# Kernel tuning notes

Measured on AMD Instinct MI355X. Metric: run time of the kernel, lower is better.

Reference implementation:

```python
import jax, jax.numpy as jnp
import numpy as np

GRID = 20            # divide = [20,20,20], hard-coded in the torch module
MIN_COORD = 10.0     # -min_voxel_coord = floor(20/2)
R = GRID * GRID * GRID  # 8000 voxels per batch element


def setup_inputs() -> dict:
    key = jax.random.key(0)
    k1, k2 = jax.random.split(key)
    B, C, N = 16, 64, 65536
    features = jax.random.normal(k1, (B, C, N), dtype=jnp.float32)
    # points spread over roughly [-30, 30] so voxel indices cover the grid
    coords = jax.random.normal(k2, (B, N, 3), dtype=jnp.float32) * 10.0
    # search_area = 40 -> voxel_size = 40/20 = 2
    search_area = jnp.ones((B, 3), dtype=jnp.float32) * 40.0
    return {"features": features, "coords": coords, "search_area": search_area}


def reference(features, coords, search_area):
    # features: [B, C, N], coords: [B, N, 3], search_area: [B, 3]
    B, C, N = features.shape
    voxel_size = search_area / GRID                     # [B, 3]
    # coords.detach() in torch -> stop_gradient here
    disc = jnp.floor(jax.lax.stop_gradient(coords) / voxel_size[:, None, :])
    idx = (disc + MIN_COORD).astype(jnp.int32)          # [B, N, 3]
    idx = jnp.clip(idx, 0, GRID - 1)
    # flat voxel index within a batch element, then offset per batch
    flat = idx[..., 0] * (GRID * GRID) + idx[..., 1] * GRID + idx[..., 2]  # [B, N]
    seg = (flat + jnp.arange(B, dtype=jnp.int32)[:, None] * R).reshape(-1)  # [B*N]
    feat_flat = features.transpose(0, 2, 1).reshape(B * N, C)               # [B*N, C]
    sums = jax.ops.segment_sum(feat_flat, seg, num_segments=B * R)          # [B*R, C]
    counts = jax.ops.segment_sum(jnp.ones((B * N,), features.dtype), seg,
                                 num_segments=B * R)                        # [B*R]
    avg = sums / jnp.maximum(counts, 1.0)[:, None]
    # -> [B, C, X, Y, Z]
    return avg.reshape(B, GRID, GRID, GRID, C).transpose(0, 4, 1, 2, 3)
```

## Files before the change

### kernel.cpp

```cpp
#include <hip/hip_runtime.h>

#define GRID_D 20
#define RVOX   8000
#define BDIM   16
#define CDIM   64
#define NPTS   65536
#define NSEG   (BDIM * RVOX)
#define NPT_TOT (BDIM * NPTS)

#define FP_SCALE  1048576.0f
#define FP_BIAS_S 16777216.0f
#define FP_INV_S  9.5367431640625e-07f

__device__ __forceinline__ void lds_fadd64(unsigned off, unsigned long long v) {
    asm volatile("ds_add_u64 %0, %1" :: "v"(off), "v"(v));
}

__device__ __forceinline__ unsigned long long pack2(float a, float b) {
    unsigned lo = (unsigned)fmaf(a, FP_SCALE, FP_BIAS_S);
    unsigned hi = (unsigned)fmaf(b, FP_SCALE, FP_BIAS_S);
    return ((unsigned long long)hi << 32) | (unsigned long long)lo;
}

__global__ __launch_bounds__(256) void k_seg(
    const float* __restrict__ coords, const float* __restrict__ search_area,
    unsigned short* __restrict__ seg_idx, unsigned int* __restrict__ hist)
{
    int gid = blockIdx.x * 256 + threadIdx.x;
    int b = gid >> 16;
    int n = gid & (NPTS - 1);

    const float inv_grid = 1.0f / (float)GRID_D;
    float vsx = search_area[b * 3 + 0] * inv_grid;
    float vsy = search_area[b * 3 + 1] * inv_grid;
    float vsz = search_area[b * 3 + 2] * inv_grid;
    const float* cp = coords + (size_t)b * NPTS * 3 + (size_t)n * 3;
    int ix = (int)(floorf(cp[0] / vsx) + 10.0f);
    int iy = (int)(floorf(cp[1] / vsy) + 10.0f);
    int iz = (int)(floorf(cp[2] / vsz) + 10.0f);
    ix = min(max(ix, 0), GRID_D - 1);
    iy = min(max(iy, 0), GRID_D - 1);
    iz = min(max(iz, 0), GRID_D - 1);
    int flat = ix * (GRID_D * GRID_D) + iy * GRID_D + iz;
    seg_idx[gid] = (unsigned short)flat;
    atomicAdd(&hist[b * RVOX + flat], 1u);
}

__global__ __launch_bounds__(512) void k_accum2(
    const float* __restrict__ features,
    const unsigned short* __restrict__ seg_idx,
    const unsigned int* __restrict__ hist,
    float* __restrict__ out)
{
    extern __shared__ unsigned long long s64[];
    int tid = threadIdx.x;
    int cp = blockIdx.x;
    int b  = blockIdx.y;

    unsigned int* sz = (unsigned int*)s64;
    for (int i = tid; i < RVOX * 2; i += 512) sz[i] = 0u;
    __syncthreads();

    const float* fA = features + ((size_t)(b * CDIM + 2 * cp)) * NPTS;
    const float* fB = fA + NPTS;
    const unsigned short* sp = seg_idx + (size_t)b * NPTS;

    const int ITER = NPTS / (512 * 4);
    int p = tid * 4;
    ushort4 sg = *reinterpret_cast<const ushort4*>(sp + p);
    float4  va = *reinterpret_cast<const float4*>(fA + p);
    float4  vb = *reinterpret_cast<const float4*>(fB + p);
    for (int it = 0; it < ITER; ++it) {
        ushort4 sgn = sg;
        float4  van = va, vbn = vb;
        int pn = p + 2048;
        if (it + 1 < ITER) {
            sgn = *reinterpret_cast<const ushort4*>(sp + pn);
            van = *reinterpret_cast<const float4*>(fA + pn);
            vbn = *reinterpret_cast<const float4*>(fB + pn);
        }
        lds_fadd64((unsigned)sg.x * 8u, pack2(va.x, vb.x));
        lds_fadd64((unsigned)sg.y * 8u, pack2(va.y, vb.y));
        lds_fadd64((unsigned)sg.z * 8u, pack2(va.z, vb.z));
        lds_fadd64((unsigned)sg.w * 8u, pack2(va.w, vb.w));
        sg = sgn; va = van; vb = vbn; p = pn;
    }
    asm volatile("s_waitcnt lgkmcnt(0)");
    __syncthreads();

    const unsigned int* hb = hist + b * RVOX;
    float* oA = out + ((size_t)(b * CDIM + 2 * cp)) * RVOX;
    float* oB = oA + RVOX;
    for (int i = tid; i < RVOX / 4; i += 512) {
        int v = i * 4;
        uint4 h4 = *reinterpret_cast<const uint4*>(hb + v);
        float4 ra, rb;
        {
            unsigned long long w;
            float cnt, inv, t;
#define UNPACK(J, HJ, RA, RB)                                        \
            w = s64[v + J];                                          \
            cnt = (float)(HJ);                                       \
            inv = 1.0f / fmaxf(cnt, 1.0f);                           \
            t = cnt * -16.0f;                                        \
            RA = fmaf((float)(unsigned)w, FP_INV_S, t) * inv;        \
            RB = fmaf((float)(unsigned)(w >> 32), FP_INV_S, t) * inv;
            UNPACK(0, h4.x, ra.x, rb.x)
            UNPACK(1, h4.y, ra.y, rb.y)
            UNPACK(2, h4.z, ra.z, rb.z)
            UNPACK(3, h4.w, ra.w, rb.w)
#undef UNPACK
        }
        *reinterpret_cast<float4*>(oA + v) = ra;
        *reinterpret_cast<float4*>(oB + v) = rb;
    }
}

__global__ __launch_bounds__(256) void voxel_scatter(
    const float* __restrict__ features, const float* __restrict__ coords,
    const float* __restrict__ search_area, float* __restrict__ sums,
    float* __restrict__ counts)
{
    int gid = blockIdx.x * blockDim.x + threadIdx.x;
    int b = gid >> 16;
    int n = gid & (NPTS - 1);
    const float inv_grid = 1.0f / (float)GRID_D;
    float vsx = search_area[b * 3 + 0] * inv_grid;
    float vsy = search_area[b * 3 + 1] * inv_grid;
    float vsz = search_area[b * 3 + 2] * inv_grid;
    const float* cp = coords + (size_t)b * NPTS * 3 + (size_t)n * 3;
    int ix = (int)(floorf(cp[0] / vsx) + 10.0f);
    int iy = (int)(floorf(cp[1] / vsy) + 10.0f);
    int iz = (int)(floorf(cp[2] / vsz) + 10.0f);
    ix = min(max(ix, 0), GRID_D - 1);
    iy = min(max(iy, 0), GRID_D - 1);
    iz = min(max(iz, 0), GRID_D - 1);
    int flat = ix * (GRID_D * GRID_D) + iy * GRID_D + iz;
    atomicAdd(&counts[b * RVOX + flat], 1.0f);
    const float* fbase = features + (size_t)b * CDIM * NPTS + n;
    float* obase = sums + (size_t)b * CDIM * RVOX + flat;
#pragma unroll 8
    for (int c = 0; c < CDIM; ++c)
        atomicAdd(obase + (size_t)c * RVOX, fbase[(size_t)c * NPTS]);
}

__global__ __launch_bounds__(256) void voxel_finalize(
    float* __restrict__ out, const float* __restrict__ counts)
{
    int gid = blockIdx.x * blockDim.x + threadIdx.x;
    int i = gid * 4;
    int b = i / (CDIM * RVOX);
    int r = i % RVOX;
    float4 s = reinterpret_cast<float4*>(out)[gid];
    float4 cnt = reinterpret_cast<const float4*>(counts)[(b * RVOX + r) >> 2];
    s.x = s.x / fmaxf(cnt.x, 1.0f);
    s.y = s.y / fmaxf(cnt.y, 1.0f);
    s.z = s.z / fmaxf(cnt.z, 1.0f);
    s.w = s.w / fmaxf(cnt.w, 1.0f);
    reinterpret_cast<float4*>(out)[gid] = s;
}

extern "C" void kernel_launch(void* const* d_in, const int* in_sizes, int n_in,
                              void* d_out, int out_size, void* d_ws, size_t ws_size,
                              hipStream_t stream) {
    const float* features    = (const float*)d_in[0];
    const float* coords      = (const float*)d_in[1];
    const float* search_area = (const float*)d_in[2];
    float* out = (float*)d_out;

    unsigned short* seg_idx = (unsigned short*)d_ws;
    unsigned int* hist = (unsigned int*)((char*)d_ws + (size_t)NPT_TOT * sizeof(unsigned short));
    size_t need = (size_t)NPT_TOT * 2 + (size_t)NSEG * 4 + 256;

    if (ws_size >= need) {
        hipMemsetAsync(hist, 0, (size_t)NSEG * sizeof(unsigned int), stream);
        k_seg<<<NPT_TOT / 256, 256, 0, stream>>>(coords, search_area, seg_idx, hist);
        dim3 agrid(CDIM / 2, BDIM);
        k_accum2<<<agrid, 512, RVOX * sizeof(unsigned long long), stream>>>(
            features, seg_idx, hist, out);
    } else {
        float* counts = (float*)d_ws;
        hipMemsetAsync(out, 0, (size_t)out_size * sizeof(float), stream);
        hipMemsetAsync(counts, 0, (size_t)NSEG * sizeof(float), stream);
        voxel_scatter<<<NPT_TOT / 256, 256, 0, stream>>>(
            features, coords, search_area, out, counts);
        int nvec = (BDIM * CDIM * RVOX) / 4;
        voxel_finalize<<<(nvec + 255) / 256, 256, 0, stream>>>(out, counts);
    }
}
```

Before: 441.7 us.

## Split channel pairs between LDS atomics and global 64-bit atomics per block

Each block now handles two channel pairs. One pair is accumulated with fixed-point 64-bit LDS atomics as before, and the other with 64-bit global atomics into a zeroed workspace buffer, which a new finalize kernel then normalizes. This halves the block count to 256 at 1024 threads, and each block reads each point's segment index once for four channels. The cost is heavy global atomic traffic, a larger memset, and an extra kernel launch.

After: 1.070 ms. 142% more time.

```diff
diff --git a/kernel.cpp b/kernel.cpp
--- a/kernel.cpp
+++ b/kernel.cpp
@@ -7,6 +7,7 @@
 #define NPTS   65536
 #define NSEG   (BDIM * RVOX)
 #define NPT_TOT (BDIM * NPTS)
+#define NPAIR  16
 
 #define FP_SCALE  1048576.0f
 #define FP_BIAS_S 16777216.0f
@@ -46,53 +47,65 @@
     atomicAdd(&hist[b * RVOX + flat], 1u);
 }
 
-__global__ __launch_bounds__(512) void k_accum2(
+__global__ __launch_bounds__(1024) void k_hyb(
     const float* __restrict__ features,
     const unsigned short* __restrict__ seg_idx,
     const unsigned int* __restrict__ hist,
+    unsigned long long* __restrict__ gsum,
     float* __restrict__ out)
 {
     extern __shared__ unsigned long long s64[];
     int tid = threadIdx.x;
-    int cp = blockIdx.x;
-    int b  = blockIdx.y;
+    int i = blockIdx.x & (NPAIR - 1);
+    int b = blockIdx.x >> 4;
 
     unsigned int* sz = (unsigned int*)s64;
-    for (int i = tid; i < RVOX * 2; i += 512) sz[i] = 0u;
+    for (int k = tid; k < RVOX * 2; k += 1024) sz[k] = 0u;
     __syncthreads();
 
-    const float* fA = features + ((size_t)(b * CDIM + 2 * cp)) * NPTS;
+    const float* fA = features + ((size_t)(b * CDIM + 2 * i)) * NPTS;
     const float* fB = fA + NPTS;
+    const float* fC = features + ((size_t)(b * CDIM + 2 * NPAIR + 2 * i)) * NPTS;
+    const float* fD = fC + NPTS;
     const unsigned short* sp = seg_idx + (size_t)b * NPTS;
-
-    const int ITER = NPTS / (512 * 4);
+    unsigned long long* gs = gsum + ((size_t)(b * NPAIR + i)) * RVOX;
+
+    const int ITER = NPTS / (1024 * 4);
     int p = tid * 4;
     ushort4 sg = *reinterpret_cast<const ushort4*>(sp + p);
     float4  va = *reinterpret_cast<const float4*>(fA + p);
     float4  vb = *reinterpret_cast<const float4*>(fB + p);
+    float4  vc = *reinterpret_cast<const float4*>(fC + p);
+    float4  vd = *reinterpret_cast<const float4*>(fD + p);
     for (int it = 0; it < ITER; ++it) {
         ushort4 sgn = sg;
-        float4  van = va, vbn = vb;
-        int pn = p + 2048;
+        float4 van = va, vbn = vb, vcn = vc, vdn = vd;
+        int pn = p + 4096;
         if (it + 1 < ITER) {
             sgn = *reinterpret_cast<const ushort4*>(sp + pn);
             van = *reinterpret_cast<const float4*>(fA + pn);
             vbn = *reinterpret_cast<const float4*>(fB + pn);
+            vcn = *reinterpret_cast<const float4*>(fC + pn);
+            vdn = *reinterpret_cast<const float4*>(fD + pn);
         }
         lds_fadd64((unsigned)sg.x * 8u, pack2(va.x, vb.x));
         lds_fadd64((unsigned)sg.y * 8u, pack2(va.y, vb.y));
         lds_fadd64((unsigned)sg.z * 8u, pack2(va.z, vb.z));
         lds_fadd64((unsigned)sg.w * 8u, pack2(va.w, vb.w));
-        sg = sgn; va = van; vb = vbn; p = pn;
+        atomicAdd(&gs[sg.x], pack2(vc.x, vd.x));
+        atomicAdd(&gs[sg.y], pack2(vc.y, vd.y));
+        atomicAdd(&gs[sg.z], pack2(vc.z, vd.z));
+        atomicAdd(&gs[sg.w], pack2(vc.w, vd.w));
+        sg = sgn; va = van; vb = vbn; vc = vcn; vd = vdn; p = pn;
     }
     asm volatile("s_waitcnt lgkmcnt(0)");
     __syncthreads();
 
     const unsigned int* hb = hist + b * RVOX;
-    float* oA = out + ((size_t)(b * CDIM + 2 * cp)) * RVOX;
+    float* oA = out + ((size_t)(b * CDIM + 2 * i)) * RVOX;
     float* oB = oA + RVOX;
-    for (int i = tid; i < RVOX / 4; i += 512) {
-        int v = i * 4;
+    for (int k = tid; k < RVOX / 4; k += 1024) {
+        int v = k * 4;
         uint4 h4 = *reinterpret_cast<const uint4*>(hb + v);
         float4 ra, rb;
         {
@@ -116,6 +129,36 @@
     }
 }
 
+__global__ __launch_bounds__(256) void k_fin(
+    const unsigned long long* __restrict__ gsum,
+    const unsigned int* __restrict__ hist,
+    float* __restrict__ out)
+{
+    int slice = blockIdx.y;
+    int t = blockIdx.x * 256 + threadIdx.x;
+    if (t >= RVOX / 2) return;
+    int b = slice >> 4;
+    int i = slice & (NPAIR - 1);
+    int v = t * 2;
+
+    const unsigned long long* gs = gsum + (size_t)slice * RVOX;
+    const unsigned int* hb = hist + b * RVOX;
+    float* oA = out + ((size_t)(b * CDIM + 2 * NPAIR + 2 * i)) * RVOX;
+    float* oB = oA + RVOX;
+
+    unsigned long long w0 = gs[v], w1 = gs[v + 1];
+    float c0 = (float)hb[v], c1 = (float)hb[v + 1];
+    float i0 = 1.0f / fmaxf(c0, 1.0f), i1 = 1.0f / fmaxf(c1, 1.0f);
+    float t0 = c0 * -16.0f, t1 = c1 * -16.0f;
+    float2 ra, rb;
+    ra.x = fmaf((float)(unsigned)w0, FP_INV_S, t0) * i0;
+    rb.x = fmaf((float)(unsigned)(w0 >> 32), FP_INV_S, t0) * i0;
+    ra.y = fmaf((float)(unsigned)w1, FP_INV_S, t1) * i1;
+    rb.y = fmaf((float)(unsigned)(w1 >> 32), FP_INV_S, t1) * i1;
+    *reinterpret_cast<float2*>(oA + v) = ra;
+    *reinterpret_cast<float2*>(oB + v) = rb;
+}
+
 __global__ __launch_bounds__(256) void voxel_scatter(
     const float* __restrict__ features, const float* __restrict__ coords,
     const float* __restrict__ search_area, float* __restrict__ sums,
@@ -169,15 +212,19 @@
     float* out = (float*)d_out;
 
     unsigned short* seg_idx = (unsigned short*)d_ws;
-    unsigned int* hist = (unsigned int*)((char*)d_ws + (size_t)NPT_TOT * sizeof(unsigned short));
-    size_t need = (size_t)NPT_TOT * 2 + (size_t)NSEG * 4 + 256;
+    unsigned int* hist = (unsigned int*)((char*)d_ws + (size_t)NPT_TOT * 2);
+    unsigned long long* gsum =
+        (unsigned long long*)((char*)d_ws + (size_t)NPT_TOT * 2 + (size_t)NSEG * 4);
+    size_t gsum_bytes = (size_t)BDIM * NPAIR * RVOX * 8;
+    size_t need = (size_t)NPT_TOT * 2 + (size_t)NSEG * 4 + gsum_bytes + 256;
 
     if (ws_size >= need) {
-        hipMemsetAsync(hist, 0, (size_t)NSEG * sizeof(unsigned int), stream);
+        hipMemsetAsync(hist, 0, (size_t)NSEG * 4 + gsum_bytes, stream);
         k_seg<<<NPT_TOT / 256, 256, 0, stream>>>(coords, search_area, seg_idx, hist);
-        dim3 agrid(CDIM / 2, BDIM);
-        k_accum2<<<agrid, 512, RVOX * sizeof(unsigned long long), stream>>>(
-            features, seg_idx, hist, out);
+        k_hyb<<<NPAIR * BDIM, 1024, RVOX * sizeof(unsigned long long), stream>>>(
+            features, seg_idx, hist, gsum, out);
+        dim3 fgrid((RVOX / 2 + 255) / 256, BDIM * NPAIR);
+        k_fin<<<fgrid, 256, 0, stream>>>(gsum, hist, out);
     } else {
         float* counts = (float*)d_ws;
         hipMemsetAsync(out, 0, (size_t)out_size * sizeof(float), stream);
```
